# Kernel tuning notes

Hardware: AMD Instinct MI355X
Metric: run time of the kernel (lower is better)

## Reference

```python
import jax, jax.numpy as jnp
import numpy as np
from jax import lax

NUM_LAYERS = 1000
DIM = 10
BATCH = 2_000_000


def setup_inputs() -> dict:
    key = jax.random.key(0)
    kx, kw, kb = jax.random.split(key, 3)
    x = jax.random.normal(kx, (BATCH, DIM), dtype=jnp.float32)
    # torch Linear weight is [out, in]; stack all 1000 layers: [L, out, in]
    # std = 1/sqrt(DIM) keeps activation scale roughly stable across 1000 layers
    Ws = jax.random.normal(kw, (NUM_LAYERS, DIM, DIM), dtype=jnp.float32) * (DIM ** -0.5)
    bs = jax.random.normal(kb, (NUM_LAYERS, DIM), dtype=jnp.float32) * 0.01
    return {"x": x, "Ws": Ws, "bs": bs}


def reference(x, Ws, bs):
    # Sequential of 1000 Linear(10,10): h <- h @ W_l.T + b_l, no activation.
    def step(h, wb):
        W, b = wb  # W: [out, in], b: [out]
        return h @ W.T + b, None
    out, _ = lax.scan(step, x, (Ws, bs))
    return out
```

## Files before the change

### kernel.cpp

```cpp
#include <hip/hip_runtime.h>

#define NUM_LAYERS 1000
#define DIM 10
#define STRIDE 112
#define LPB 16
#define NBLK 63
#define WQ4 320
#define TILE_Q4 1280

__device__ inline void gload_lds16(const void* g, void* l) {
    __builtin_amdgcn_global_load_lds(
        (const __attribute__((address_space(1))) void*)g,
        (__attribute__((address_space(3))) void*)l, 16, 0, 0);
}

__device__ inline void compose_one(const float* __restrict__ src,
                                   float* __restrict__ dst,
                                   int c, int lane) {
    const float* F = src + (size_t)(2 * c) * STRIDE;
    const float* G = src + (size_t)(2 * c + 1) * STRIDE;
    float colf[DIM], o[DIM];
    #pragma unroll
    for (int r = 0; r < DIM; ++r) colf[r] = F[lane * DIM + r];
    #pragma unroll
    for (int r = 0; r < DIM; ++r) {
        float acc = (lane == DIM) ? G[100 + r] : 0.f;
        #pragma unroll
        for (int k = 0; k < DIM; ++k)
            acc += G[k * DIM + r] * colf[k];
        o[r] = acc;
    }
    float* D = dst + (size_t)c * STRIDE;
    #pragma unroll
    for (int r = 0; r < DIM; ++r) D[lane * DIM + r] = o[r];
}

__global__ __launch_bounds__(1024) void compose16(const float* __restrict__ Ws,
                                                  const float* __restrict__ bs,
                                                  float* __restrict__ wsout) {
    __shared__ float A[LPB * STRIDE];
    __shared__ float B[(LPB / 2) * STRIDE];
    const int tid = threadIdx.x;
    const int blk = blockIdx.x;

    for (int e = tid; e < LPB * 100; e += 1024) {
        int ll = e / 100, rem = e % 100;
        int r = rem / 10, k = rem % 10;
        int l = blk * LPB + ll;
        float v = (l < NUM_LAYERS) ? Ws[(size_t)l * 100 + rem]
                                   : (r == k ? 1.f : 0.f);
        A[ll * STRIDE + k * DIM + r] = v;
    }
    for (int e = tid; e < LPB * DIM; e += 1024) {
        int ll = e / DIM, r = e % DIM;
        int l = blk * LPB + ll;
        float v = (l < NUM_LAYERS) ? bs[(size_t)l * DIM + r] : 0.f;
        A[ll * STRIDE + 100 + r] = v;
    }

    const int wave = tid >> 6, lane = tid & 63;
    const float* src = A;
    float* dst = B;
    for (int n = LPB / 2; n >= 1; n >>= 1) {
        __syncthreads();
        if (wave < n && lane <= DIM) compose_one(src, dst, wave, lane);
        const float* t = dst; dst = (float*)src; src = t;
    }
    __syncthreads();
    if (tid < 110) wsout[(size_t)blk * STRIDE + tid] = A[tid];
}

__global__ __launch_bounds__(1024) void compose_tree64(const float* __restrict__ wsin,
                                                       float* __restrict__ aff) {
    __shared__ float A[64 * STRIDE];
    __shared__ float B[32 * STRIDE];
    const int tid = threadIdx.x;

    for (int e = tid; e < 64 * STRIDE; e += 1024) {
        int chunk = e / STRIDE, pos = e % STRIDE;
        float v;
        if (pos >= 110)        v = 0.f;
        else if (chunk < NBLK) v = wsin[(size_t)chunk * STRIDE + pos];
        else v = (pos < 100 && (pos / 10 == pos % 10)) ? 1.f : 0.f;
        A[e] = v;
    }

    const int wave = tid >> 6, lane = tid & 63;
    const float* src = A;
    float* dst = B;
    for (int n = 32; n >= 1; n >>= 1) {
        __syncthreads();
        if (lane <= DIM)
            for (int c = wave; c < n; c += 16)
                compose_one(src, dst, c, lane);
        const float* t = dst; dst = (float*)src; src = t;
    }
    __syncthreads();
    if (tid < 110) {
        if (tid < 100) {
            int j = tid / DIM, r = tid % DIM;
            aff[r * DIM + j] = A[tid];
        } else {
            aff[tid] = A[tid];
        }
    }
}

__global__ __launch_bounds__(256) void apply_affine(const float* __restrict__ x,
                                                    const float* __restrict__ aff,
                                                    float* __restrict__ out,
                                                    int nq4) {
    __shared__ float4 lds4[4][WQ4];
    __shared__ float4 s4[28];
    const int tid  = threadIdx.x;
    const int w    = tid >> 6, lane = tid & 63;
    const float* __restrict__ s = (const float*)s4;

    const int q0 = blockIdx.x * TILE_Q4 + w * WQ4;
    const int rem = nq4 - q0;
    if (rem <= 0) return;

    if (lane < 28) s4[lane] = ((const float4*)aff)[lane];

    const float4* __restrict__ xin = (const float4*)x + q0;
    float4* __restrict__ op = (float4*)out + q0;

    #pragma unroll
    for (int i = 0; i < 5; ++i) {
        int q = i * 64 + lane;
        gload_lds16(xin + (q < rem ? q : 0), &lds4[w][i * 64]);
    }

    asm volatile("s_waitcnt vmcnt(0) lgkmcnt(0)" ::: "memory");
    __builtin_amdgcn_sched_barrier(0);

    float xv[20];
    #pragma unroll
    for (int i = 0; i < 5; ++i) {
        float4 v = lds4[w][5 * lane + i];
        xv[4*i+0] = v.x; xv[4*i+1] = v.y; xv[4*i+2] = v.z; xv[4*i+3] = v.w;
    }

    float o[20];
    #pragma unroll
    for (int rr = 0; rr < 2; ++rr)
        #pragma unroll
        for (int j = 0; j < DIM; ++j) {
            float acc = s[100 + j];
            #pragma unroll
            for (int k = 0; k < DIM; ++k)
                acc += s[j * DIM + k] * xv[rr * DIM + k];
            o[rr * DIM + j] = acc;
        }

    #pragma unroll
    for (int i = 0; i < 5; ++i)
        lds4[w][5 * lane + i] = make_float4(o[4*i+0], o[4*i+1], o[4*i+2], o[4*i+3]);

    asm volatile("s_waitcnt lgkmcnt(0)" ::: "memory");
    __builtin_amdgcn_sched_barrier(0);

    {
        float4 t0 = lds4[w][0 * 64 + lane];
        float4 t1 = lds4[w][1 * 64 + lane];
        float4 t2 = lds4[w][2 * 64 + lane];
        float4 t3 = lds4[w][3 * 64 + lane];
        float4 t4 = lds4[w][4 * 64 + lane];
        if (0 * 64 + lane < rem) op[0 * 64 + lane] = t0;
        if (1 * 64 + lane < rem) op[1 * 64 + lane] = t1;
        if (2 * 64 + lane < rem) op[2 * 64 + lane] = t2;
        if (3 * 64 + lane < rem) op[3 * 64 + lane] = t3;
        if (4 * 64 + lane < rem) op[4 * 64 + lane] = t4;
    }
}

extern "C" void kernel_launch(void* const* d_in, const int* in_sizes, int n_in,
                              void* d_out, int out_size, void* d_ws, size_t ws_size,
                              hipStream_t stream) {
    const float* x  = (const float*)d_in[0];
    const float* Ws = (const float*)d_in[1];
    const float* bs = (const float*)d_in[2];
    float* out = (float*)d_out;

    float* ws_chunks = (float*)d_ws;
    float* ws_aff    = ws_chunks + NBLK * STRIDE;

    compose16<<<NBLK, 1024, 0, stream>>>(Ws, bs, ws_chunks);
    compose_tree64<<<1, 1024, 0, stream>>>(ws_chunks, ws_aff);

    const int nq4 = in_sizes[0] / 4;
    const int blocks = (nq4 + TILE_Q4 - 1) / TILE_Q4;
    apply_affine<<<blocks, 256, 0, stream>>>(x, ws_aff, out, nq4);
}
```

Baseline: 165.1 us.

## Fold final 8-chunk composition into apply kernel, dropping the single-block tree launch

The layer-composition stage now uses 8 blocks of 125 layers each instead of 63 blocks of 16 followed by a single-block 64-way tree kernel. The last 8-to-1 composition is redone redundantly by wave 0 of every apply block, while the other waves spin on an LDS flag, overlapping with the x prefetch into LDS. This removes one kernel launch and its serial single-block stage. In exchange every apply block does extra compose work, and each compose128 block runs a deeper 7-level reduction.

```diff
diff --git a/kernel.cpp b/kernel.cpp
--- a/kernel.cpp
+++ b/kernel.cpp
@@ -3,8 +3,9 @@
 #define NUM_LAYERS 1000
 #define DIM 10
 #define STRIDE 112
-#define LPB 16
-#define NBLK 63
+#define LPB128 128
+#define REAL125 125
+#define NCH8 8
 #define WQ4 320
 #define TILE_Q4 1280
 
@@ -14,9 +15,7 @@
         (__attribute__((address_space(3))) void*)l, 16, 0, 0);
 }
 
-__device__ inline void compose_one(const float* __restrict__ src,
-                                   float* __restrict__ dst,
-                                   int c, int lane) {
+__device__ inline void compose_one(const float* src, float* dst, int c, int lane) {
     const float* F = src + (size_t)(2 * c) * STRIDE;
     const float* G = src + (size_t)(2 * c + 1) * STRIDE;
     float colf[DIM], o[DIM];
@@ -35,60 +34,30 @@
     for (int r = 0; r < DIM; ++r) D[lane * DIM + r] = o[r];
 }
 
-__global__ __launch_bounds__(1024) void compose16(const float* __restrict__ Ws,
-                                                  const float* __restrict__ bs,
-                                                  float* __restrict__ wsout) {
-    __shared__ float A[LPB * STRIDE];
-    __shared__ float B[(LPB / 2) * STRIDE];
-    const int tid = threadIdx.x;
-    const int blk = blockIdx.x;
+__global__ __launch_bounds__(1024) void compose128(const float* __restrict__ Ws,
+                                                   const float* __restrict__ bs,
+                                                   float* __restrict__ wsout) {
+    __shared__ float A[LPB128 * STRIDE];
+    __shared__ float B[64 * STRIDE];
+    const int tid = threadIdx.x, blk = blockIdx.x;
 
-    for (int e = tid; e < LPB * 100; e += 1024) {
+    for (int e = tid; e < LPB128 * 100; e += 1024) {
         int ll = e / 100, rem = e % 100;
         int r = rem / 10, k = rem % 10;
-        int l = blk * LPB + ll;
-        float v = (l < NUM_LAYERS) ? Ws[(size_t)l * 100 + rem]
-                                   : (r == k ? 1.f : 0.f);
+        float v = (ll < REAL125) ? Ws[(size_t)(blk * REAL125 + ll) * 100 + rem]
+                                 : (r == k ? 1.f : 0.f);
         A[ll * STRIDE + k * DIM + r] = v;
     }
-    for (int e = tid; e < LPB * DIM; e += 1024) {
+    for (int e = tid; e < LPB128 * DIM; e += 1024) {
         int ll = e / DIM, r = e % DIM;
-        int l = blk * LPB + ll;
-        float v = (l < NUM_LAYERS) ? bs[(size_t)l * DIM + r] : 0.f;
+        float v = (ll < REAL125) ? bs[(size_t)(blk * REAL125 + ll) * DIM + r] : 0.f;
         A[ll * STRIDE + 100 + r] = v;
     }
 
     const int wave = tid >> 6, lane = tid & 63;
     const float* src = A;
     float* dst = B;
-    for (int n = LPB / 2; n >= 1; n >>= 1) {
-        __syncthreads();
-        if (wave < n && lane <= DIM) compose_one(src, dst, wave, lane);
-        const float* t = dst; dst = (float*)src; src = t;
-    }
-    __syncthreads();
-    if (tid < 110) wsout[(size_t)blk * STRIDE + tid] = A[tid];
-}
-
-__global__ __launch_bounds__(1024) void compose_tree64(const float* __restrict__ wsin,
-                                                       float* __restrict__ aff) {
-    __shared__ float A[64 * STRIDE];
-    __shared__ float B[32 * STRIDE];
-    const int tid = threadIdx.x;
-
-    for (int e = tid; e < 64 * STRIDE; e += 1024) {
-        int chunk = e / STRIDE, pos = e % STRIDE;
-        float v;
-        if (pos >= 110)        v = 0.f;
-        else if (chunk < NBLK) v = wsin[(size_t)chunk * STRIDE + pos];
-        else v = (pos < 100 && (pos / 10 == pos % 10)) ? 1.f : 0.f;
-        A[e] = v;
-    }
-
-    const int wave = tid >> 6, lane = tid & 63;
-    const float* src = A;
-    float* dst = B;
-    for (int n = 32; n >= 1; n >>= 1) {
+    for (int n = 64; n >= 1; n >>= 1) {
         __syncthreads();
         if (lane <= DIM)
             for (int c = wave; c < n; c += 16)
@@ -96,40 +65,64 @@
         const float* t = dst; dst = (float*)src; src = t;
     }
     __syncthreads();
-    if (tid < 110) {
-        if (tid < 100) {
-            int j = tid / DIM, r = tid % DIM;
-            aff[r * DIM + j] = A[tid];
-        } else {
-            aff[tid] = A[tid];
-        }
-    }
+    if (tid < 110) wsout[(size_t)blk * STRIDE + tid] = src[tid];
 }
 
-__global__ __launch_bounds__(256) void apply_affine(const float* __restrict__ x,
-                                                    const float* __restrict__ aff,
-                                                    float* __restrict__ out,
-                                                    int nq4) {
+__global__ __launch_bounds__(256) void apply_fold(const float* __restrict__ x,
+                                                  const float* __restrict__ chunks,
+                                                  float* __restrict__ out,
+                                                  int nq4) {
     __shared__ float4 lds4[4][WQ4];
-    __shared__ float4 s4[28];
+    __shared__ float FC[12 * STRIDE];
+    __shared__ int fold_flag;
     const int tid  = threadIdx.x;
     const int w    = tid >> 6, lane = tid & 63;
-    const float* __restrict__ s = (const float*)s4;
+
+    if (tid == 0) fold_flag = 0;
+    __syncthreads();
 
     const int q0 = blockIdx.x * TILE_Q4 + w * WQ4;
     const int rem = nq4 - q0;
-    if (rem <= 0) return;
-
-    if (lane < 28) s4[lane] = ((const float4*)aff)[lane];
+    if (w != 0 && rem <= 0) return;
 
     const float4* __restrict__ xin = (const float4*)x + q0;
     float4* __restrict__ op = (float4*)out + q0;
 
-    #pragma unroll
-    for (int i = 0; i < 5; ++i) {
-        int q = i * 64 + lane;
-        gload_lds16(xin + (q < rem ? q : 0), &lds4[w][i * 64]);
+    if (rem > 0) {
+        #pragma unroll
+        for (int i = 0; i < 5; ++i) {
+            int q = i * 64 + lane;
+            gload_lds16(xin + (q < rem ? q : 0), &lds4[w][i * 64]);
+        }
     }
+
+    if (w == 0) {
+        const float4* c4 = (const float4*)chunks;
+        float4* F4 = (float4*)FC;
+        #pragma unroll
+        for (int i = 0; i < 4; ++i) {
+            int e = i * 64 + lane;
+            if (e < NCH8 * (STRIDE / 4)) F4[e] = c4[e];
+        }
+        asm volatile("s_waitcnt vmcnt(0) lgkmcnt(0)" ::: "memory");
+        __builtin_amdgcn_sched_barrier(0);
+
+        const int c = lane >> 4, sub = lane & 15;
+        if (sub <= DIM) compose_one(FC, FC + 8 * STRIDE, c, sub);
+        asm volatile("s_waitcnt lgkmcnt(0)" ::: "memory");
+        __builtin_amdgcn_sched_barrier(0);
+        if (c < 2 && sub <= DIM) compose_one(FC + 8 * STRIDE, FC, c, sub);
+        asm volatile("s_waitcnt lgkmcnt(0)" ::: "memory");
+        __builtin_amdgcn_sched_barrier(0);
+        if (c == 0 && sub <= DIM) compose_one(FC, FC + 2 * STRIDE, 0, sub);
+        asm volatile("s_waitcnt lgkmcnt(0)" ::: "memory");
+        __builtin_amdgcn_sched_barrier(0);
+        if (lane == 0) *(volatile int*)&fold_flag = 1;
+    } else {
+        while (*(volatile int*)&fold_flag == 0) __builtin_amdgcn_s_sleep(2);
+    }
+
+    const float* s = FC + 2 * STRIDE;
 
     asm volatile("s_waitcnt vmcnt(0) lgkmcnt(0)" ::: "memory");
     __builtin_amdgcn_sched_barrier(0);
@@ -149,7 +142,7 @@
             float acc = s[100 + j];
             #pragma unroll
             for (int k = 0; k < DIM; ++k)
-                acc += s[j * DIM + k] * xv[rr * DIM + k];
+                acc += s[k * DIM + j] * xv[rr * DIM + k];
             o[rr * DIM + j] = acc;
         }
 
@@ -183,12 +176,10 @@
     float* out = (float*)d_out;
 
     float* ws_chunks = (float*)d_ws;
-    float* ws_aff    = ws_chunks + NBLK * STRIDE;
 
-    compose16<<<NBLK, 1024, 0, stream>>>(Ws, bs, ws_chunks);
-    compose_tree64<<<1, 1024, 0, stream>>>(ws_chunks, ws_aff);
+    compose128<<<NCH8, 1024, 0, stream>>>(Ws, bs, ws_chunks);
 
     const int nq4 = in_sizes[0] / 4;
     const int blocks = (nq4 + TILE_Q4 - 1) / TILE_Q4;
-    apply_affine<<<blocks, 256, 0, stream>>>(x, ws_aff, out, nq4);
+    apply_fold<<<blocks, 256, 0, stream>>>(x, ws_chunks, out, nq4);
 }
```

Measured after the change: 180.9 us. 9.6% more time.
